# Performance work log

Hardware: AMD Instinct MI355X
Metric: run time of the kernel (lower is better)

The kernel has to match this reference:

```python
import jax, jax.numpy as jnp
import numpy as np

VOCAB, HID = 32000, 1024
SEQ, BATCH = 64, 32

def setup_inputs() -> dict:
    key = jax.random.key(0)
    ks = jax.random.split(key, 12)
    w = 0.1  # winit uniform(-winit, winit)
    u = lambda k, shape: jax.random.uniform(k, shape, jnp.float32, -w, w)
    return {
        "x": jax.random.randint(ks[0], (SEQ, BATCH), 0, VOCAB),
        "emb_W": u(ks[1], (VOCAB, HID)),
        "Wx0": u(ks[2], (4 * HID, HID)), "Wh0": u(ks[3], (4 * HID, HID)),
        "bx0": u(ks[4], (4 * HID,)), "bh0": u(ks[5], (4 * HID,)),
        "Wx1": u(ks[6], (4 * HID, HID)), "Wh1": u(ks[7], (4 * HID, HID)),
        "bx1": u(ks[8], (4 * HID,)), "bh1": u(ks[9], (4 * HID,)),
        "fc_W": u(ks[10], (VOCAB, HID)), "fc_b": u(ks[11], (VOCAB,)),
        "h0": jnp.zeros((BATCH, HID), jnp.float32),
        "c0": jnp.zeros((BATCH, HID), jnp.float32),
        "h1": jnp.zeros((BATCH, HID), jnp.float32),
        "c1": jnp.zeros((BATCH, HID), jnp.float32),
    }

def _lstm_layer(inp, h, c, Wx, Wh, bx, bh):
    # inp: [T, B, H]; h, c: [B, H]
    def step(carry, x_t):
        h, c = carry
        gx = x_t @ Wx.T + bx      # [B, 4H]
        gh = h @ Wh.T + bh        # [B, 4H]
        xi, xf, xo, xn = jnp.split(gx, 4, axis=1)
        hi, hf, ho, hn = jnp.split(gh, 4, axis=1)
        i = jax.nn.sigmoid(xi + hi)
        f = jax.nn.sigmoid(xf + hf)
        o = jax.nn.sigmoid(xo + ho)
        n = jnp.tanh(xn + hn)
        c = f * c + i * n
        h = o * jnp.tanh(c)
        return (h, c), h
    (h, c), ys = jax.lax.scan(step, (h, c), inp)
    return ys, h, c

def reference(x, emb_W, Wx0, Wh0, bx0, bh0, Wx1, Wh1, bx1, bh1,
              fc_W, fc_b, h0, c0, h1, c1):
    e = emb_W[x]                                   # [T, B, H] embedding gather
    y0, h0f, c0f = _lstm_layer(e, h0, c0, Wx0, Wh0, bx0, bh0)
    y1, h1f, c1f = _lstm_layer(y0, h1, c1, Wx1, Wh1, bx1, bh1)
    # Linear.forward flattens to [T*B, H] then projects to vocab (dropout=0)
    logits = y1.reshape(-1, y1.shape[-1]) @ fc_W.T + fc_b  # [T*B, V]
    return logits, h0f, c0f, h1f, c1f
```

## Files before the change

kernel.cpp:

```cpp
#include <hip/hip_runtime.h>
#include <hip/hip_bf16.h>
#include <stdint.h>

typedef __bf16 bf16x8 __attribute__((ext_vector_type(8)));
typedef float  f32x4  __attribute__((ext_vector_type(4)));

#define HID   1024
#define SEQT  64
#define BATCH 32
#define GATES 4096
#define ROWS  2048
#define VOCAB 32000
#define HSLAB (64 * 32 * 16)
#define AGT __HIP_MEMORY_SCOPE_AGENT

__device__ __forceinline__ unsigned short f2bf(float f) {
    union { float f; unsigned u; } v; v.f = f;
    unsigned u = v.u + 0x7FFFu + ((v.u >> 16) & 1u);
    return (unsigned short)(u >> 16);
}

__device__ __forceinline__ float sigm(float x) { return 1.f / (1.f + expf(-x)); }

__device__ __forceinline__ void gload_lds16(const void* g, void* l) {
    __builtin_amdgcn_global_load_lds(
        (const __attribute__((address_space(1))) unsigned int*)g,
        (__attribute__((address_space(3))) unsigned int*)l,
        16, 0, 0);
}

__device__ __forceinline__ ushort4 cvt4(float4 v) {
    ushort4 o;
    o.x = f2bf(v.x); o.y = f2bf(v.y); o.z = f2bf(v.z); o.w = f2bf(v.w);
    return o;
}

__global__ __launch_bounds__(256) void prologue_k(
    const int* __restrict__ x, const float* __restrict__ embW,
    unsigned short* __restrict__ eb,
    const float* __restrict__ Wx0, unsigned short* __restrict__ Wx0b,
    const float* __restrict__ h0, const float* __restrict__ h1,
    unsigned short* __restrict__ h0b, unsigned short* __restrict__ h1b,
    int* __restrict__ bar)
{
    const int bid = blockIdx.x, tid = threadIdx.x;
    const float4* src = (const float4*)(embW + (size_t)x[bid] * HID);
    ((ushort4*)(eb + (size_t)bid * HID))[tid] = cvt4(src[tid]);
    int base = bid * 512 + tid;
    ((ushort4*)Wx0b)[base]       = cvt4(((const float4*)Wx0)[base]);
    ((ushort4*)Wx0b)[base + 256] = cvt4(((const float4*)Wx0)[base + 256]);
    int i = bid * 256 + tid;
    if (i < 32768) {
        int blk = i >> 9, b = (i >> 4) & 31, w = i & 15;
        int col = blk * 16 + w;
        h0b[i] = f2bf(h0[b * HID + col]);
        h1b[i] = f2bf(h1[b * HID + col]);
        if (i < 8192) bar[i] = 0;
    }
}

__global__ __launch_bounds__(256) void gemm_bt(
    const unsigned short* __restrict__ A,
    const unsigned short* __restrict__ B,
    float* __restrict__ C,
    const float* __restrict__ bias0,
    const float* __restrict__ bias1,
    int M, int N, int K)
{
    __shared__ unsigned short As[128][32];
    __shared__ unsigned short Bs[128][32];
    const int tid  = threadIdx.x;
    const int lane = tid & 63;
    const int wr   = (tid >> 7) & 1;
    const int wc   = (tid >> 6) & 1;

    const int nmp = M >> 7, nnp = N >> 7;
    const int nwg = nmp * nnp, per = nwg >> 3;
    const int wid = (blockIdx.x & 7) * per + (blockIdx.x >> 3);
    const int bm  = (wid % nmp) << 7;
    const int bn  = (wid / nmp) << 7;

    const int lr   = lane & 15;
    const int lk   = (lane >> 4) * 8;

    f32x4 acc[4][4];
    #pragma unroll
    for (int m = 0; m < 4; ++m)
        #pragma unroll
        for (int n = 0; n < 4; ++n) acc[m][n] = 0.f;

    for (int kt = 0; kt < K; kt += 32) {
        __syncthreads();
        #pragma unroll
        for (int i = 0; i < 2; ++i) {
            int ch = tid + i * 256;
            int r = ch >> 2, c8 = (ch & 3) * 8;
            gload_lds16(A + (size_t)(bm + r) * K + kt + c8, (char*)&As[0][0] + ch * 16);
            gload_lds16(B + (size_t)(bn + r) * K + kt + c8, (char*)&Bs[0][0] + ch * 16);
        }
        __syncthreads();
        bf16x8 af[4], bfr[4];
        #pragma unroll
        for (int m = 0; m < 4; ++m)
            af[m] = *(const bf16x8*)&As[wr * 64 + m * 16 + lr][lk];
        #pragma unroll
        for (int n = 0; n < 4; ++n)
            bfr[n] = *(const bf16x8*)&Bs[wc * 64 + n * 16 + lr][lk];
        #pragma unroll
        for (int m = 0; m < 4; ++m)
            #pragma unroll
            for (int n = 0; n < 4; ++n)
                acc[m][n] = __builtin_amdgcn_mfma_f32_16x16x32_bf16(af[m], bfr[n], acc[m][n], 0, 0, 0);
    }

    const int row0 = bm + wr * 64, col0 = bn + wc * 64;
    #pragma unroll
    for (int n = 0; n < 4; ++n) {
        int col = col0 + n * 16 + lr;
        float badd = 0.f;
        if (bias0) badd += bias0[col];
        if (bias1) badd += bias1[col];
        #pragma unroll
        for (int m = 0; m < 4; ++m) {
            #pragma unroll
            for (int j = 0; j < 4; ++j) {
                int row = row0 + m * 16 + (lane >> 4) * 4 + j;
                C[(size_t)row * N + col] = acc[m][n][j] + badd;
            }
        }
    }
}

__global__ __launch_bounds__(256, 1) void lstm_fused_k(
    const float* __restrict__ Wh0f,
    const float* __restrict__ Wx1f,
    const float* __restrict__ Wh1f,
    const float* __restrict__ gx0,
    const float* __restrict__ bx1,
    const float* __restrict__ bh1,
    const unsigned short* __restrict__ h0b,
    const unsigned short* __restrict__ h1b,
    const float* __restrict__ c0i,
    const float* __restrict__ c1i,
    unsigned short* __restrict__ y0x,
    unsigned short* __restrict__ y1x,
    float* __restrict__ part,
    float* __restrict__ h0f, float* __restrict__ c0f,
    float* __restrict__ h1f, float* __restrict__ c1f,
    int* __restrict__ bar,
    const float* __restrict__ fcW,
    unsigned short* __restrict__ fcWb)
{
    const int tid  = threadIdx.x;
    const int bid  = blockIdx.x;
    const int xcd  = bid & 7;
    const int role = xcd >> 1;
    const int wg   = ((bid >> 3) << 1) | (xcd & 1);

    if (role == 3) {
        int base = wg * 256 + tid;
        const float4* f4 = (const float4*)fcW;
        uint4* o4 = (uint4*)fcWb;
        const int n8 = VOCAB * HID / 8;
        for (int i = base; i < n8; i += 16384) {
            float4 v0 = f4[2 * i], v1 = f4[2 * i + 1];
            uint4 o;
            o.x = (unsigned)f2bf(v0.x) | ((unsigned)f2bf(v0.y) << 16);
            o.y = (unsigned)f2bf(v0.z) | ((unsigned)f2bf(v0.w) << 16);
            o.z = (unsigned)f2bf(v1.x) | ((unsigned)f2bf(v1.y) << 16);
            o.w = (unsigned)f2bf(v1.z) | ((unsigned)f2bf(v1.w) << 16);
            o4[i] = o;
        }
        return;
    }

    __builtin_amdgcn_fence(__ATOMIC_ACQUIRE, "agent");

    __shared__ char smem[65536 + 8192];
    float* pre = (float*)(smem + 65536);
    const int lane = tid & 63;
    const int wave = tid >> 6;
    const int lr   = lane & 15;
    const int lk8  = (lane >> 4) * 8;
    const int r0   = lr, r1 = 16 + lr;
    const int kby  = (lane >> 4) * 16;
    const int eb_  = tid >> 3;
    const int ecp  = (tid & 7) * 2;
    const int ecol = wg * 16 + ecp;

    bf16x8 wf[32];
    {
        const float* Wsrc = (role == 0) ? Wh0f : (role == 1) ? Wx1f : Wh1f;
        const float* p = Wsrc + (size_t)(wave * HID + wg * 16 + lr) * HID + lk8;
        #pragma unroll
        for (int kk = 0; kk < 32; ++kk) {
            float4 v0 = *(const float4*)(p + kk * 32);
            float4 v1 = *(const float4*)(p + kk * 32 + 4);
            union { bf16x8 v; unsigned short s[8]; } u;
            u.s[0] = f2bf(v0.x); u.s[1] = f2bf(v0.y);
            u.s[2] = f2bf(v0.z); u.s[3] = f2bf(v0.w);
            u.s[4] = f2bf(v1.x); u.s[5] = f2bf(v1.y);
            u.s[6] = f2bf(v1.z); u.s[7] = f2bf(v1.w);
            wf[kk] = u.v;
        }
        #pragma unroll
        for (int kk = 0; kk < 32; ++kk) asm volatile("" : "+v"(wf[kk]));
    }

    auto stage_g = [&](const unsigned short* src) {
        #pragma unroll
        for (int j = 0; j < 16; ++j) {
            int base = wave * 16384 + j * 1024;
            int d = base + lane * 16;
            int r = d >> 11;
            int cb = (d & 2047) ^ ((r & 7) << 4);
            int e0 = cb >> 1;
            int g = (((e0 >> 4) * 32 + r) * 16 + (e0 & 15)) * 2;
            gload_lds16((const char*)src + g, smem + base);
        }
    };
    auto mm = [&](f32x4& A0, f32x4& A1) {
        #pragma unroll
        for (int kk = 0; kk < 32; ++kk) {
            int k2 = kk * 64 + kby;
            bf16x8 x0 = *(const bf16x8*)(smem + r0 * 2048 + (k2 ^ ((r0 & 7) << 4)));
            bf16x8 x1 = *(const bf16x8*)(smem + r1 * 2048 + (k2 ^ ((r1 & 7) << 4)));
            A0 = __builtin_amdgcn_mfma_f32_16x16x32_bf16(x0, wf[kk], A0, 0, 0, 0);
            A1 = __builtin_amdgcn_mfma_f32_16x16x32_bf16(x1, wf[kk], A1, 0, 0, 0);
        }
    };
    auto spill = [&](const f32x4& a0, const f32x4& a1) {
        float* pg = pre + wave * 512;
        #pragma unroll
        for (int j = 0; j < 4; ++j) {
            pg[((lane >> 4) * 4 + j) * 16 + lr]        = a0[j];
            pg[((lane >> 4) * 4 + j + 16) * 16 + lr]   = a1[j];
        }
    };
    auto pollge = [&](int grp, int val) {
        for (;;) {
            int f = __hip_atomic_load(&bar[(grp * 64 + lane) * 32],
                                      __ATOMIC_RELAXED, AGT);
            if (__all(f >= val)) break;
            __builtin_amdgcn_s_sleep(1);
        }
    };

    if (role == 0) {
        float creg0, creg1;
        { float2 c2 = *(const float2*)&c0i[eb_ * HID + ecol]; creg0 = c2.x; creg1 = c2.y; }
        for (int t = 0; t < SEQT; ++t) {
            float2 gpre[4];
            const float* gxr = gx0 + (size_t)(t * BATCH + eb_) * GATES + ecol;
            #pragma unroll
            for (int g = 0; g < 4; ++g) gpre[g] = *(const float2*)(gxr + g * HID);
            if (t > 0) pollge(0, t);
            asm volatile("" ::: "memory");
            stage_g(t == 0 ? h0b : y0x + (size_t)(t - 1) * HSLAB);
            __syncthreads();
            f32x4 a0 = 0.f, a1 = 0.f;
            mm(a0, a1);
            spill(a0, a1);
            __syncthreads();
            float2 P[4];
            #pragma unroll
            for (int g = 0; g < 4; ++g) {
                float2 pr = *(const float2*)&pre[(g * 32 + eb_) * 16 + ecp];
                P[g].x = pr.x + gpre[g].x; P[g].y = pr.y + gpre[g].y;
            }
            float i0 = sigm(P[0].x), fg0 = sigm(P[1].x), o0 = sigm(P[2].x), n0 = tanhf(P[3].x);
            float i1 = sigm(P[0].y), fg1 = sigm(P[1].y), o1 = sigm(P[2].y), n1 = tanhf(P[3].y);
            float cn0 = fg0 * creg0 + i0 * n0, cn1 = fg1 * creg1 + i1 * n1;
            float hv0 = o0 * tanhf(cn0), hv1 = o1 * tanhf(cn1);
            creg0 = cn0; creg1 = cn1;
            unsigned pk = (unsigned)f2bf(hv0) | ((unsigned)f2bf(hv1) << 16);
            __hip_atomic_store(
                (unsigned*)&y0x[(size_t)t * HSLAB + (wg * 32 + eb_) * 16 + ecp],
                pk, __ATOMIC_RELAXED, AGT);
            if (t == SEQT - 1) {
                *(float2*)&h0f[eb_ * HID + ecol] = make_float2(hv0, hv1);
                *(float2*)&c0f[eb_ * HID + ecol] = make_float2(cn0, cn1);
            }
            __syncthreads();
            if (tid == 0)
                __hip_atomic_store(&bar[wg * 32], t + 1, __ATOMIC_RELAXED, AGT);
        }
    } else if (role == 1) {
        for (int t = 0; t < SEQT; ++t) {
            pollge(0, t + 1);
            asm volatile("" ::: "memory");
            stage_g(y0x + (size_t)t * HSLAB);
            __syncthreads();
            f32x4 a0 = 0.f, a1 = 0.f;
            mm(a0, a1);
            {
                float* pb = part + (((size_t)(t * 4 + wave) * 64 + wg) * 32) * 16;
                int brow = (lane >> 4) * 4;
                #pragma unroll
                for (int j = 0; j < 4; ++j) {
                    __hip_atomic_store(pb + (brow + j) * 16 + lr,      a0[j],
                                       __ATOMIC_RELAXED, AGT);
                    __hip_atomic_store(pb + (brow + j + 16) * 16 + lr, a1[j],
                                       __ATOMIC_RELAXED, AGT);
                }
            }
            __syncthreads();
            if (tid == 0)
                __hip_atomic_store(&bar[(64 + wg) * 32], t + 1, __ATOMIC_RELAXED, AGT);
        }
    } else {
        float creg0, creg1;
        { float2 c2 = *(const float2*)&c1i[eb_ * HID + ecol]; creg0 = c2.x; creg1 = c2.y; }
        float2 b1r[4];
        #pragma unroll
        for (int g = 0; g < 4; ++g) {
            float2 a = *(const float2*)&bx1[g * HID + ecol];
            float2 b = *(const float2*)&bh1[g * HID + ecol];
            b1r[g].x = a.x + b.x; b1r[g].y = a.y + b.y;
        }
        for (int t = 0; t < SEQT; ++t) {
            pollge(1, t + 1);
            if (t > 0) pollge(2, t);
            asm volatile("" ::: "memory");
            stage_g(t == 0 ? h1b : y1x + (size_t)(t - 1) * HSLAB);
            __syncthreads();
            f32x4 a0 = 0.f, a1 = 0.f;
            mm(a0, a1);
            spill(a0, a1);
            __syncthreads();
            float2 P[4];
            #pragma unroll
            for (int g = 0; g < 4; ++g) {
                float2 pr = *(const float2*)&pre[(g * 32 + eb_) * 16 + ecp];
                float2 px = *(const float2*)(part +
                    ((((size_t)(t * 4 + g) * 64 + wg) * 32 + eb_) * 16 + ecp));
                P[g].x = pr.x + px.x + b1r[g].x;
                P[g].y = pr.y + px.y + b1r[g].y;
            }
            float i0 = sigm(P[0].x), fg0 = sigm(P[1].x), o0 = sigm(P[2].x), n0 = tanhf(P[3].x);
            float i1 = sigm(P[0].y), fg1 = sigm(P[1].y), o1 = sigm(P[2].y), n1 = tanhf(P[3].y);
            float cn0 = fg0 * creg0 + i0 * n0, cn1 = fg1 * creg1 + i1 * n1;
            float hv0 = o0 * tanhf(cn0), hv1 = o1 * tanhf(cn1);
            creg0 = cn0; creg1 = cn1;
            unsigned pk = (unsigned)f2bf(hv0) | ((unsigned)f2bf(hv1) << 16);
            __hip_atomic_store(
                (unsigned*)&y1x[(size_t)t * HSLAB + (wg * 32 + eb_) * 16 + ecp],
                pk, __ATOMIC_RELAXED, AGT);
            if (t == SEQT - 1) {
                *(float2*)&h1f[eb_ * HID + ecol] = make_float2(hv0, hv1);
                *(float2*)&c1f[eb_ * HID + ecol] = make_float2(cn0, cn1);
            }
            __syncthreads();
            if (tid == 0)
                __hip_atomic_store(&bar[(128 + wg) * 32], t + 1, __ATOMIC_RELAXED, AGT);
        }
    }
}

__global__ __launch_bounds__(512) void fc_k(
    const unsigned short* __restrict__ y1x,
    const unsigned short* __restrict__ fcWb,
    const float* __restrict__ fcb,
    float* __restrict__ logits)
{
    __shared__ unsigned short As[256 * 64];
    __shared__ unsigned short Bs[128 * 64];
    const int tid  = threadIdx.x;
    const int lane = tid & 63;
    const int wave = tid >> 6;
    const int wr   = wave >> 1;
    const int wc   = wave & 1;
    const int lr   = lane & 15;
    const int lk2  = (lane >> 4) * 16;

    const int per = 2000 >> 3;
    const int wid = ((int)blockIdx.x & 7) * per + ((int)blockIdx.x >> 3);
    const int bm  = (wid & 7) << 8;
    const int bn  = (wid >> 3) << 7;

    f32x4 acc[4][4];
    #pragma unroll
    for (int m = 0; m < 4; ++m)
        #pragma unroll
        for (int n = 0; n < 4; ++n) acc[m][n] = 0.f;

    for (int kt = 0; kt < HID; kt += 64) {
        __syncthreads();
        #pragma unroll
        for (int i = 0; i < 4; ++i) {
            int ch = tid + i * 512;
            int row = ch >> 3, ck = ch & 7;
            int R = bm + row;
            int e = kt + ((ck ^ (row & 7)) << 3);
            const char* asrc = (const char*)y1x +
                ((((size_t)(R >> 5) * 64 + (e >> 4)) * 32 + (R & 31)) * 16 + (e & 15)) * 2;
            gload_lds16(asrc, (char*)As + ch * 16);
        }
        #pragma unroll
        for (int i = 0; i < 2; ++i) {
            int ch = tid + i * 512;
            int row = ch >> 3, ck = ch & 7;
            int e = kt + ((ck ^ (row & 7)) << 3);
            gload_lds16(fcWb + (size_t)(bn + row) * HID + e, (char*)Bs + ch * 16);
        }
        __syncthreads();
        #pragma unroll
        for (int kh = 0; kh < 2; ++kh) {
            bf16x8 af[4], bfr[4];
            #pragma unroll
            for (int m = 0; m < 4; ++m) {
                int row = wr * 64 + m * 16 + lr;
                af[m] = *(const bf16x8*)((char*)As + row * 128 +
                         ((kh * 64 + lk2) ^ ((row & 7) << 4)));
            }
            #pragma unroll
            for (int n = 0; n < 4; ++n) {
                int row = wc * 64 + n * 16 + lr;
                bfr[n] = *(const bf16x8*)((char*)Bs + row * 128 +
                         ((kh * 64 + lk2) ^ ((row & 7) << 4)));
            }
            #pragma unroll
            for (int m = 0; m < 4; ++m)
                #pragma unroll
                for (int n = 0; n < 4; ++n)
                    acc[m][n] = __builtin_amdgcn_mfma_f32_16x16x32_bf16(
                        af[m], bfr[n], acc[m][n], 0, 0, 0);
        }
    }

    const int row0 = bm + wr * 64, col0 = bn + wc * 64;
    #pragma unroll
    for (int n = 0; n < 4; ++n) {
        int col = col0 + n * 16 + lr;
        float badd = fcb[col];
        #pragma unroll
        for (int m = 0; m < 4; ++m) {
            #pragma unroll
            for (int j = 0; j < 4; ++j) {
                int row = row0 + m * 16 + (lane >> 4) * 4 + j;
                logits[(size_t)row * VOCAB + col] = acc[m][n][j] + badd;
            }
        }
    }
}

extern "C" void kernel_launch(void* const* d_in, const int* in_sizes, int n_in,
                              void* d_out, int out_size, void* d_ws, size_t ws_size,
                              hipStream_t stream) {
    const int*   x    = (const int*)d_in[0];
    const float* embW = (const float*)d_in[1];
    const float* Wx0  = (const float*)d_in[2];
    const float* Wh0  = (const float*)d_in[3];
    const float* bx0  = (const float*)d_in[4];
    const float* bh0  = (const float*)d_in[5];
    const float* Wx1  = (const float*)d_in[6];
    const float* Wh1  = (const float*)d_in[7];
    const float* bx1  = (const float*)d_in[8];
    const float* bh1  = (const float*)d_in[9];
    const float* fcW  = (const float*)d_in[10];
    const float* fcb  = (const float*)d_in[11];
    const float* h0   = (const float*)d_in[12];
    const float* c0   = (const float*)d_in[13];
    const float* h1   = (const float*)d_in[14];
    const float* c1   = (const float*)d_in[15];

    char* ws = (char*)d_ws;
    size_t off = 0;
    auto alloc = [&](size_t bytes) {
        char* p = ws + off;
        off += (bytes + 255) & ~(size_t)255;
        return p;
    };
    unsigned short* eb    = (unsigned short*)alloc((size_t)ROWS * HID * 2);
    unsigned short* Wx0b  = (unsigned short*)alloc((size_t)GATES * HID * 2);
    unsigned short* fcWb  = (unsigned short*)alloc((size_t)VOCAB * HID * 2);
    float*          gx0   = (float*)alloc((size_t)ROWS * GATES * 4);
    float*          part  = (float*)alloc((size_t)SEQT * 4 * 64 * 32 * 16 * 4);
    unsigned short* y0x   = (unsigned short*)alloc((size_t)SEQT * HSLAB * 2);
    unsigned short* y1x   = (unsigned short*)alloc((size_t)SEQT * HSLAB * 2);
    unsigned short* h0b   = (unsigned short*)alloc((size_t)BATCH * HID * 2);
    unsigned short* h1b   = (unsigned short*)alloc((size_t)BATCH * HID * 2);
    int*            bar   = (int*)alloc((size_t)256 * 32 * 4);
    (void)ws_size; (void)in_sizes; (void)n_in; (void)out_size;

    float* logits = (float*)d_out;
    float* h0f = logits + (size_t)ROWS * VOCAB;
    float* c0f = h0f + BATCH * HID;
    float* h1f = c0f + BATCH * HID;
    float* c1f = h1f + BATCH * HID;

    prologue_k<<<ROWS, 256, 0, stream>>>(x, embW, eb, Wx0, Wx0b,
                                         h0, h1, h0b, h1b, bar);
    gemm_bt<<<(ROWS / 128) * (GATES / 128), 256, 0, stream>>>(
        eb, Wx0b, gx0, bx0, bh0, ROWS, GATES, HID);
    lstm_fused_k<<<256, 256, 0, stream>>>(Wh0, Wx1, Wh1, gx0, bx1, bh1,
                                          h0b, h1b, c0, c1, y0x, y1x, part,
                                          h0f, c0f, h1f, c1f, bar, fcW, fcWb);
    fc_k<<<2000, 512, 0, stream>>>(y1x, fcWb, fcb, logits);
}
```

Before: 544.5 us.

## Interleave gate weight rows so each lane holds all four gates in registers

Reorders the recurrent weight rows for the layer-0 and layer-1 recurrence roles so that each MFMA output lane holds the i, f, o and n gates for one hidden column. The operands are swapped so the accumulator layout matches this. The LDS spill of preactivations and the extra __syncthreads per timestep go away, and the elementwise LSTM update reads accumulators directly. It also moves the layer-1 partial-sum loads before the staging step. The cost is narrower scalar 16-bit atomic stores and scalar gx loads instead of packed float2 accesses.

```diff
diff --git a/kernel.cpp b/kernel.cpp
--- a/kernel.cpp
+++ b/kernel.cpp
@@ -177,21 +177,19 @@
     __builtin_amdgcn_fence(__ATOMIC_ACQUIRE, "agent");
 
     __shared__ char smem[65536 + 8192];
-    float* pre = (float*)(smem + 65536);
     const int lane = tid & 63;
     const int wave = tid >> 6;
     const int lr   = lane & 15;
     const int lk8  = (lane >> 4) * 8;
     const int r0   = lr, r1 = 16 + lr;
     const int kby  = (lane >> 4) * 16;
-    const int eb_  = tid >> 3;
-    const int ecp  = (tid & 7) * 2;
-    const int ecol = wg * 16 + ecp;
 
     bf16x8 wf[32];
     {
         const float* Wsrc = (role == 0) ? Wh0f : (role == 1) ? Wx1f : Wh1f;
-        const float* p = Wsrc + (size_t)(wave * HID + wg * 16 + lr) * HID + lk8;
+        const int wrow = (role == 1) ? (wave * 1024 + wg * 16 + lr)
+                                     : ((lr & 3) * 1024 + wg * 16 + wave * 4 + (lr >> 2));
+        const float* p = Wsrc + (size_t)wrow * HID + lk8;
         #pragma unroll
         for (int kk = 0; kk < 32; ++kk) {
             float4 v0 = *(const float4*)(p + kk * 32);
@@ -219,7 +217,17 @@
             gload_lds16((const char*)src + g, smem + base);
         }
     };
-    auto mm = [&](f32x4& A0, f32x4& A1) {
+    auto mmA = [&](f32x4& A0, f32x4& A1) {
+        #pragma unroll
+        for (int kk = 0; kk < 32; ++kk) {
+            int k2 = kk * 64 + kby;
+            bf16x8 x0 = *(const bf16x8*)(smem + r0 * 2048 + (k2 ^ ((r0 & 7) << 4)));
+            bf16x8 x1 = *(const bf16x8*)(smem + r1 * 2048 + (k2 ^ ((r1 & 7) << 4)));
+            A0 = __builtin_amdgcn_mfma_f32_16x16x32_bf16(wf[kk], x0, A0, 0, 0, 0);
+            A1 = __builtin_amdgcn_mfma_f32_16x16x32_bf16(wf[kk], x1, A1, 0, 0, 0);
+        }
+    };
+    auto mmB = [&](f32x4& A0, f32x4& A1) {
         #pragma unroll
         for (int kk = 0; kk < 32; ++kk) {
             int k2 = kk * 64 + kby;
@@ -227,14 +235,6 @@
             bf16x8 x1 = *(const bf16x8*)(smem + r1 * 2048 + (k2 ^ ((r1 & 7) << 4)));
             A0 = __builtin_amdgcn_mfma_f32_16x16x32_bf16(x0, wf[kk], A0, 0, 0, 0);
             A1 = __builtin_amdgcn_mfma_f32_16x16x32_bf16(x1, wf[kk], A1, 0, 0, 0);
-        }
-    };
-    auto spill = [&](const f32x4& a0, const f32x4& a1) {
-        float* pg = pre + wave * 512;
-        #pragma unroll
-        for (int j = 0; j < 4; ++j) {
-            pg[((lane >> 4) * 4 + j) * 16 + lr]        = a0[j];
-            pg[((lane >> 4) * 4 + j + 16) * 16 + lr]   = a1[j];
         }
     };
     auto pollge = [&](int grp, int val) {
@@ -246,40 +246,44 @@
         }
     };
 
+    const int b0  = lane & 15, b1 = b0 + 16;
+    const int cl  = lane >> 4;
+    const int col = wg * 16 + wave * 4 + cl;
+    const int w   = wave * 4 + cl;
+
     if (role == 0) {
-        float creg0, creg1;
-        { float2 c2 = *(const float2*)&c0i[eb_ * HID + ecol]; creg0 = c2.x; creg1 = c2.y; }
+        float creg0 = c0i[b0 * HID + col];
+        float creg1 = c0i[b1 * HID + col];
         for (int t = 0; t < SEQT; ++t) {
-            float2 gpre[4];
-            const float* gxr = gx0 + (size_t)(t * BATCH + eb_) * GATES + ecol;
-            #pragma unroll
-            for (int g = 0; g < 4; ++g) gpre[g] = *(const float2*)(gxr + g * HID);
+            float gp0[4], gp1[4];
+            const float* gxr = gx0 + (size_t)t * BATCH * GATES + col;
+            #pragma unroll
+            for (int g = 0; g < 4; ++g) {
+                gp0[g] = gxr[(size_t)b0 * GATES + g * HID];
+                gp1[g] = gxr[(size_t)b1 * GATES + g * HID];
+            }
             if (t > 0) pollge(0, t);
             asm volatile("" ::: "memory");
             stage_g(t == 0 ? h0b : y0x + (size_t)(t - 1) * HSLAB);
             __syncthreads();
             f32x4 a0 = 0.f, a1 = 0.f;
-            mm(a0, a1);
-            spill(a0, a1);
-            __syncthreads();
-            float2 P[4];
-            #pragma unroll
-            for (int g = 0; g < 4; ++g) {
-                float2 pr = *(const float2*)&pre[(g * 32 + eb_) * 16 + ecp];
-                P[g].x = pr.x + gpre[g].x; P[g].y = pr.y + gpre[g].y;
-            }
-            float i0 = sigm(P[0].x), fg0 = sigm(P[1].x), o0 = sigm(P[2].x), n0 = tanhf(P[3].x);
-            float i1 = sigm(P[0].y), fg1 = sigm(P[1].y), o1 = sigm(P[2].y), n1 = tanhf(P[3].y);
-            float cn0 = fg0 * creg0 + i0 * n0, cn1 = fg1 * creg1 + i1 * n1;
-            float hv0 = o0 * tanhf(cn0), hv1 = o1 * tanhf(cn1);
-            creg0 = cn0; creg1 = cn1;
-            unsigned pk = (unsigned)f2bf(hv0) | ((unsigned)f2bf(hv1) << 16);
+            mmA(a0, a1);
+            float i0 = sigm(a0[0] + gp0[0]), fg0 = sigm(a0[1] + gp0[1]);
+            float o0 = sigm(a0[2] + gp0[2]), n0 = tanhf(a0[3] + gp0[3]);
+            float i1 = sigm(a1[0] + gp1[0]), fg1 = sigm(a1[1] + gp1[1]);
+            float o1 = sigm(a1[2] + gp1[2]), n1 = tanhf(a1[3] + gp1[3]);
+            creg0 = fg0 * creg0 + i0 * n0;
+            creg1 = fg1 * creg1 + i1 * n1;
+            float hv0 = o0 * tanhf(creg0), hv1 = o1 * tanhf(creg1);
             __hip_atomic_store(
-                (unsigned*)&y0x[(size_t)t * HSLAB + (wg * 32 + eb_) * 16 + ecp],
-                pk, __ATOMIC_RELAXED, AGT);
+                &y0x[(size_t)t * HSLAB + (wg * 32 + b0) * 16 + w],
+                f2bf(hv0), __ATOMIC_RELAXED, AGT);
+            __hip_atomic_store(
+                &y0x[(size_t)t * HSLAB + (wg * 32 + b1) * 16 + w],
+                f2bf(hv1), __ATOMIC_RELAXED, AGT);
             if (t == SEQT - 1) {
-                *(float2*)&h0f[eb_ * HID + ecol] = make_float2(hv0, hv1);
-                *(float2*)&c0f[eb_ * HID + ecol] = make_float2(cn0, cn1);
+                h0f[b0 * HID + col] = hv0;  h0f[b1 * HID + col] = hv1;
+                c0f[b0 * HID + col] = creg0; c0f[b1 * HID + col] = creg1;
             }
             __syncthreads();
             if (tid == 0)
@@ -292,7 +296,7 @@
             stage_g(y0x + (size_t)t * HSLAB);
             __syncthreads();
             f32x4 a0 = 0.f, a1 = 0.f;
-            mm(a0, a1);
+            mmB(a0, a1);
             {
                 float* pb = part + (((size_t)(t * 4 + wave) * 64 + wg) * 32) * 16;
                 int brow = (lane >> 4) * 4;
@@ -309,46 +313,43 @@
                 __hip_atomic_store(&bar[(64 + wg) * 32], t + 1, __ATOMIC_RELAXED, AGT);
         }
     } else {
-        float creg0, creg1;
-        { float2 c2 = *(const float2*)&c1i[eb_ * HID + ecol]; creg0 = c2.x; creg1 = c2.y; }
-        float2 b1r[4];
-        #pragma unroll
-        for (int g = 0; g < 4; ++g) {
-            float2 a = *(const float2*)&bx1[g * HID + ecol];
-            float2 b = *(const float2*)&bh1[g * HID + ecol];
-            b1r[g].x = a.x + b.x; b1r[g].y = a.y + b.y;
-        }
+        float creg0 = c1i[b0 * HID + col];
+        float creg1 = c1i[b1 * HID + col];
+        float br[4];
+        #pragma unroll
+        for (int g = 0; g < 4; ++g)
+            br[g] = bx1[g * HID + col] + bh1[g * HID + col];
         for (int t = 0; t < SEQT; ++t) {
             pollge(1, t + 1);
             if (t > 0) pollge(2, t);
             asm volatile("" ::: "memory");
+            float px0[4], px1[4];
+            #pragma unroll
+            for (int g = 0; g < 4; ++g) {
+                const float* pb = part + ((size_t)(t * 4 + g) * 64 + wg) * 512;
+                px0[g] = pb[b0 * 16 + w];
+                px1[g] = pb[b1 * 16 + w];
+            }
             stage_g(t == 0 ? h1b : y1x + (size_t)(t - 1) * HSLAB);
             __syncthreads();
             f32x4 a0 = 0.f, a1 = 0.f;
-            mm(a0, a1);
-            spill(a0, a1);
-            __syncthreads();
-            float2 P[4];
-            #pragma unroll
-            for (int g = 0; g < 4; ++g) {
-                float2 pr = *(const float2*)&pre[(g * 32 + eb_) * 16 + ecp];
-                float2 px = *(const float2*)(part +
-                    ((((size_t)(t * 4 + g) * 64 + wg) * 32 + eb_) * 16 + ecp));
-                P[g].x = pr.x + px.x + b1r[g].x;
-                P[g].y = pr.y + px.y + b1r[g].y;
-            }
-            float i0 = sigm(P[0].x), fg0 = sigm(P[1].x), o0 = sigm(P[2].x), n0 = tanhf(P[3].x);
-            float i1 = sigm(P[0].y), fg1 = sigm(P[1].y), o1 = sigm(P[2].y), n1 = tanhf(P[3].y);
-            float cn0 = fg0 * creg0 + i0 * n0, cn1 = fg1 * creg1 + i1 * n1;
-            float hv0 = o0 * tanhf(cn0), hv1 = o1 * tanhf(cn1);
-            creg0 = cn0; creg1 = cn1;
-            unsigned pk = (unsigned)f2bf(hv0) | ((unsigned)f2bf(hv1) << 16);
+            mmA(a0, a1);
+            float i0 = sigm(a0[0] + px0[0] + br[0]), fg0 = sigm(a0[1] + px0[1] + br[1]);
+            float o0 = sigm(a0[2] + px0[2] + br[2]), n0 = tanhf(a0[3] + px0[3] + br[3]);
+            float i1 = sigm(a1[0] + px1[0] + br[0]), fg1 = sigm(a1[1] + px1[1] + br[1]);
+            float o1 = sigm(a1[2] + px1[2] + br[2]), n1 = tanhf(a1[3] + px1[3] + br[3]);
+            creg0 = fg0 * creg0 + i0 * n0;
+            creg1 = fg1 * creg1 + i1 * n1;
+            float hv0 = o0 * tanhf(creg0), hv1 = o1 * tanhf(creg1);
             __hip_atomic_store(
-                (unsigned*)&y1x[(size_t)t * HSLAB + (wg * 32 + eb_) * 16 + ecp],
-                pk, __ATOMIC_RELAXED, AGT);
+                &y1x[(size_t)t * HSLAB + (wg * 32 + b0) * 16 + w],
+                f2bf(hv0), __ATOMIC_RELAXED, AGT);
+            __hip_atomic_store(
+                &y1x[(size_t)t * HSLAB + (wg * 32 + b1) * 16 + w],
+                f2bf(hv1), __ATOMIC_RELAXED, AGT);
             if (t == SEQT - 1) {
-                *(float2*)&h1f[eb_ * HID + ecol] = make_float2(hv0, hv1);
-                *(float2*)&c1f[eb_ * HID + ecol] = make_float2(cn0, cn1);
+                h1f[b0 * HID + col] = hv0;  h1f[b1 * HID + col] = hv1;
+                c1f[b0 * HID + col] = creg0; c1f[b1 * HID + col] = creg1;
             }
             __syncthreads();
             if (tid == 0)
```

Result: slower. 642.6 us (+18.0%).
